# Kernel tuning notes

Hardware: AMD Instinct MI355X
Metric: run time of the kernel (lower is better)

The kernel has to match this reference:

```python
import jax, jax.numpy as jnp
import numpy as np

THRESHOLD = 0.5

def setup_inputs() -> dict:
    key = jax.random.key(0)
    x = jax.random.normal(key, (32, 2048, 1024), dtype=jnp.float32)
    return {"x": x}

def reference(x) -> jnp.ndarray:
    # x: [B, S, D]
    B, S, D = x.shape
    x_centered = x - jnp.mean(x, axis=1, keepdims=True)          # [B, S, D]
    # per-sample covariance: [B, D, D]
    cov = jnp.einsum('bsd,bse->bde', x_centered, x_centered) / (S - 1)
    std = jnp.sqrt(jnp.diagonal(cov, axis1=1, axis2=2))          # [B, D]
    corr = cov / (std[:, :, None] * std[:, None, :])             # [B, D, D]
    mask = jnp.abs(corr) > THRESHOLD                             # [B, D, D]
    eye = jnp.eye(D, dtype=bool)
    mask = mask & ~eye                                           # zero the diagonal
    # torch semantics: output[b, :, j] = 0 for every masked (b, i, j)
    col_kill = jnp.any(mask, axis=1)                             # [B, D]
    return x * (~col_kill)[:, None, :].astype(x.dtype)
```

## Files before the change

kernel.cpp:

```cpp
#include <hip/hip_runtime.h>
#include <stdint.h>

#define B_ 32
#define S_ 2048
#define D_ 1024

typedef __attribute__((ext_vector_type(16))) float f32x16;

__device__ __forceinline__ void async_copy16(const void* g, void* l) {
  __builtin_amdgcn_global_load_lds(
      (const __attribute__((address_space(1))) uint32_t*)g,
      (__attribute__((address_space(3))) uint32_t*)l, 16, 0, 0);
}

__device__ __forceinline__ int row_off(int m, int ch) {
  return m * 128 + ((ch ^ (m & 7)) << 4);
}

template <bool COPY>
__global__ __launch_bounds__(256) void prepass_kernel(const float* __restrict__ x,
                                                      uint8_t* __restrict__ xt,
                                                      float2* __restrict__ part,
                                                      float* __restrict__ out) {
  __shared__ float s_s[256 * 4];
  __shared__ float s_q[256 * 4];
  int dt = blockIdx.x;
  int slab = blockIdx.y;
  int b = blockIdx.z;
  int t = threadIdx.x;
  int q = t & 31;
  int e = t >> 5;
  int g = e >> 1, bh = e & 1;

  const size_t base = ((size_t)b * S_ + (size_t)slab * 128 + g * 32 + bh * 8) * D_ +
                      dt * 128 + q * 4;
  const float* xb = x + base;
  float4 r[16];
#pragma unroll
  for (int j = 0; j < 8; ++j) r[j] = *(const float4*)(xb + (size_t)j * D_);
#pragma unroll
  for (int j = 0; j < 8; ++j) r[8 + j] = *(const float4*)(xb + (size_t)(16 + j) * D_);

  if (COPY) {
    float* ob = out + base;
#pragma unroll
    for (int j = 0; j < 8; ++j) *(float4*)(ob + (size_t)j * D_) = r[j];
#pragma unroll
    for (int j = 0; j < 8; ++j) *(float4*)(ob + (size_t)(16 + j) * D_) = r[8 + j];
  }

  uint8_t* img = xt + (((size_t)b * 8 + dt) * 16 + slab) * 16384;
#pragma unroll
  for (int c = 0; c < 4; ++c) {
    float v[16];
#pragma unroll
    for (int j = 0; j < 16; ++j) v[j] = ((const float*)&r[j])[c];
    float ps = 0.f, pq = 0.f;
#pragma unroll
    for (int j = 0; j < 16; ++j) { ps += v[j]; pq += v[j] * v[j]; }
    s_s[t * 4 + c] = ps;
    s_q[t * 4 + c] = pq;
    uint32_t w0 = 0, w1 = 0, w2 = 0, w3 = 0;
    w0 = __builtin_amdgcn_cvt_pk_fp8_f32(v[0], v[1], w0, false);
    w0 = __builtin_amdgcn_cvt_pk_fp8_f32(v[2], v[3], w0, true);
    w1 = __builtin_amdgcn_cvt_pk_fp8_f32(v[4], v[5], w1, false);
    w1 = __builtin_amdgcn_cvt_pk_fp8_f32(v[6], v[7], w1, true);
    w2 = __builtin_amdgcn_cvt_pk_fp8_f32(v[8], v[9], w2, false);
    w2 = __builtin_amdgcn_cvt_pk_fp8_f32(v[10], v[11], w2, true);
    w3 = __builtin_amdgcn_cvt_pk_fp8_f32(v[12], v[13], w3, false);
    w3 = __builtin_amdgcn_cvt_pk_fp8_f32(v[14], v[15], w3, true);
    int m = 4 * q + c;
    *(uint4*)(img + row_off(m, (g << 1) | bh)) = make_uint4(w0, w1, w2, w3);
  }
  __syncthreads();
  if (t < 128) {
    int m = t, qq = m >> 2, cc = m & 3;
    float ss = 0.f, sq = 0.f;
#pragma unroll
    for (int ee = 0; ee < 8; ++ee) {
      ss += s_s[(qq + 32 * ee) * 4 + cc];
      sq += s_q[(qq + 32 * ee) * 4 + cc];
    }
    part[(size_t)slab * 32768 + b * 1024 + dt * 128 + m] = make_float2(ss, sq);
  }
}

__global__ void finalize_kernel(const float2* __restrict__ part,
                                float* __restrict__ meanB,
                                float* __restrict__ stdB) {
  int i = blockIdx.x * 256 + threadIdx.x;
  float s = 0.f, qv = 0.f;
#pragma unroll
  for (int sl = 0; sl < 16; ++sl) {
    float2 p = part[(size_t)sl * 32768 + i];
    s += p.x;
    qv += p.y;
  }
  float m = s * (1.0f / (float)S_);
  float var = (qv - s * m) * (1.0f / (float)(S_ - 1));
  meanB[i] = m;
  stdB[i] = sqrtf(fmaxf(var, 0.f));
}

__global__ __launch_bounds__(256) void gram_kernel(const uint8_t* __restrict__ xt,
                                                   const float* __restrict__ meanB,
                                                   const float* __restrict__ stdB,
                                                   int* __restrict__ colkill) {
  __shared__ uint8_t smA[16384];
  __shared__ uint8_t smB[16384];
  int b = blockIdx.y;
  int p = blockIdx.x;
  int i = 0;
  while (p >= 8 - i) { p -= 8 - i; ++i; }
  int j = i + p;

  int tid = threadIdx.x;
  int lane = tid & 63, wave = tid >> 6;
  int wm = wave & 1, wn = wave >> 1;
  int l31 = lane & 31, half = lane >> 5;

  f32x16 acc[2][2];
#pragma unroll
  for (int a = 0; a < 2; ++a)
#pragma unroll
    for (int c = 0; c < 2; ++c)
#pragma unroll
      for (int r = 0; r < 16; ++r) acc[a][c][r] = 0.f;

  const uint8_t* gA = xt + ((size_t)b * 8 + i) * 262144;
  const uint8_t* gB = xt + ((size_t)b * 8 + j) * 262144;
  bool diag = (i == j);

  for (int sl = 0; sl < 16; ++sl) {
    __syncthreads();
    const uint8_t* srcA = gA + (size_t)sl * 16384;
    for (int c = wave; c < 16; c += 4)
      async_copy16(srcA + c * 1024 + lane * 16, (void*)(smA + c * 1024));
    if (!diag) {
      const uint8_t* srcB = gB + (size_t)sl * 16384;
      for (int c = wave; c < 16; c += 4)
        async_copy16(srcB + c * 1024 + lane * 16, (void*)(smB + c * 1024));
    }
    __syncthreads();

    const uint8_t* bA = smA;
    const uint8_t* bB = diag ? smA : smB;
#pragma unroll
    for (int g = 0; g < 4; ++g) {
      ulonglong2 a0 = *(const ulonglong2*)(bA + row_off(wm * 64 + l31, (g << 1) | half));
      ulonglong2 a1 = *(const ulonglong2*)(bA + row_off(wm * 64 + 32 + l31, (g << 1) | half));
      ulonglong2 b0 = *(const ulonglong2*)(bB + row_off(wn * 64 + l31, (g << 1) | half));
      ulonglong2 b1 = *(const ulonglong2*)(bB + row_off(wn * 64 + 32 + l31, (g << 1) | half));
      acc[0][0] = __builtin_amdgcn_mfma_f32_32x32x16_fp8_fp8((long)a0.x, (long)b0.x, acc[0][0], 0, 0, 0);
      acc[0][1] = __builtin_amdgcn_mfma_f32_32x32x16_fp8_fp8((long)a0.x, (long)b1.x, acc[0][1], 0, 0, 0);
      acc[1][0] = __builtin_amdgcn_mfma_f32_32x32x16_fp8_fp8((long)a1.x, (long)b0.x, acc[1][0], 0, 0, 0);
      acc[1][1] = __builtin_amdgcn_mfma_f32_32x32x16_fp8_fp8((long)a1.x, (long)b1.x, acc[1][1], 0, 0, 0);
      acc[0][0] = __builtin_amdgcn_mfma_f32_32x32x16_fp8_fp8((long)a0.y, (long)b0.y, acc[0][0], 0, 0, 0);
      acc[0][1] = __builtin_amdgcn_mfma_f32_32x32x16_fp8_fp8((long)a0.y, (long)b1.y, acc[0][1], 0, 0, 0);
      acc[1][0] = __builtin_amdgcn_mfma_f32_32x32x16_fp8_fp8((long)a1.y, (long)b0.y, acc[1][0], 0, 0, 0);
      acc[1][1] = __builtin_amdgcn_mfma_f32_32x32x16_fp8_fp8((long)a1.y, (long)b1.y, acc[1][1], 0, 0, 0);
    }
  }

  const float* mb = meanB + b * D_;
  const float* sb = stdB + b * D_;
#pragma unroll
  for (int t = 0; t < 2; ++t) {
#pragma unroll
    for (int u = 0; u < 2; ++u) {
      int e = j * 128 + wn * 64 + u * 32 + l31;
      float me = mb[e], se05 = 0.5f * sb[e];
#pragma unroll
      for (int r = 0; r < 16; ++r) {
        int row = half * 4 + (r & 3) + 8 * (r >> 2);
        int d = i * 128 + wm * 64 + t * 32 + row;
        float cov = (acc[t][u][r] - (float)S_ * mb[d] * me) * (1.0f / (float)(S_ - 1));
        if (d != e && fabsf(cov) > se05 * sb[d]) {
          atomicOr(colkill + b * D_ + e, 1);
          atomicOr(colkill + b * D_ + d, 1);
        }
      }
    }
  }
}

__global__ void apply_kernel(const float* __restrict__ x,
                             const int* __restrict__ colkill,
                             float* __restrict__ out) {
  size_t idx = (size_t)blockIdx.x * 256 + threadIdx.x;
  const float4 v = ((const float4*)x)[idx];
  size_t e0 = idx * 4;
  int d = (int)(e0 & (D_ - 1));
  int b = (int)(e0 >> 21);
  const int4 k = *(const int4*)(colkill + b * D_ + d);
  float4 o;
  o.x = k.x ? 0.f : v.x;
  o.y = k.y ? 0.f : v.y;
  o.z = k.z ? 0.f : v.z;
  o.w = k.w ? 0.f : v.w;
  ((float4*)out)[idx] = o;
}

__global__ __launch_bounds__(256) void zerocol_kernel(const int* __restrict__ colkill,
                                                      float* __restrict__ out) {
  int bd = blockIdx.x * 256 + threadIdx.x;
  if (colkill[bd] == 0) return;
  int b = bd >> 10, d = bd & (D_ - 1);
  float* p = out + (size_t)b * S_ * D_ + d;
#pragma unroll 8
  for (int s = 0; s < S_; ++s) p[(size_t)s * D_] = 0.f;
}

extern "C" void kernel_launch(void* const* d_in, const int* in_sizes, int n_in,
                              void* d_out, int out_size, void* d_ws, size_t ws_size,
                              hipStream_t stream) {
  const float* x = (const float*)d_in[0];
  float* out = (float*)d_out;

  const size_t need = ((size_t)69 << 20);
  if (ws_size >= need) {
    uint8_t* xt = (uint8_t*)d_ws;
    float2* part = (float2*)((uint8_t*)d_ws + ((size_t)64 << 20));
    float* meanB = (float*)((uint8_t*)d_ws + ((size_t)68 << 20));
    float* stdB = meanB + 32768;
    int* colkill = (int*)(stdB + 32768);

    hipMemsetAsync(colkill, 0, 32768 * sizeof(int), stream);
    prepass_kernel<true><<<dim3(8, 16, 32), 256, 0, stream>>>(x, xt, part, out);
    finalize_kernel<<<128, 256, 0, stream>>>(part, meanB, stdB);
    gram_kernel<<<dim3(36, 32), 256, 0, stream>>>(xt, meanB, stdB, colkill);
    zerocol_kernel<<<128, 256, 0, stream>>>(colkill, out);
  } else {
    uint8_t* xt = (uint8_t*)d_out;
    float2* part = (float2*)d_ws;
    float* meanB = (float*)((uint8_t*)d_ws + (16 * 32768) * sizeof(float2));
    float* stdB = meanB + 32768;
    int* colkill = (int*)(stdB + 32768);

    hipMemsetAsync(colkill, 0, 32768 * sizeof(int), stream);
    prepass_kernel<false><<<dim3(8, 16, 32), 256, 0, stream>>>(x, xt, part, nullptr);
    finalize_kernel<<<128, 256, 0, stream>>>(part, meanB, stdB);
    gram_kernel<<<dim3(36, 32), 256, 0, stream>>>(xt, meanB, stdB, colkill);
    apply_kernel<<<65536, 256, 0, stream>>>(x, colkill, out);
  }
}
```

Before: 529.3 us.

## Double-buffer gram LDS loads, fuse stats finalize into gram, use nontemporal prepass I/O

```diff
diff --git a/kernel.cpp b/kernel.cpp
--- a/kernel.cpp
+++ b/kernel.cpp
@@ -6,6 +6,7 @@
 #define D_ 1024
 
 typedef __attribute__((ext_vector_type(16))) float f32x16;
+typedef __attribute__((ext_vector_type(4))) float f32x4;
 
 __device__ __forceinline__ void async_copy16(const void* g, void* l) {
   __builtin_amdgcn_global_load_lds(
@@ -34,19 +35,21 @@
 
   const size_t base = ((size_t)b * S_ + (size_t)slab * 128 + g * 32 + bh * 8) * D_ +
                       dt * 128 + q * 4;
-  const float* xb = x + base;
-  float4 r[16];
-#pragma unroll
-  for (int j = 0; j < 8; ++j) r[j] = *(const float4*)(xb + (size_t)j * D_);
-#pragma unroll
-  for (int j = 0; j < 8; ++j) r[8 + j] = *(const float4*)(xb + (size_t)(16 + j) * D_);
+  const f32x4* xb = (const f32x4*)(x + base);
+  f32x4 r[16];
+#pragma unroll
+  for (int j = 0; j < 8; ++j) r[j] = __builtin_nontemporal_load(xb + (size_t)j * (D_ / 4));
+#pragma unroll
+  for (int j = 0; j < 8; ++j)
+    r[8 + j] = __builtin_nontemporal_load(xb + (size_t)(16 + j) * (D_ / 4));
 
   if (COPY) {
-    float* ob = out + base;
-#pragma unroll
-    for (int j = 0; j < 8; ++j) *(float4*)(ob + (size_t)j * D_) = r[j];
-#pragma unroll
-    for (int j = 0; j < 8; ++j) *(float4*)(ob + (size_t)(16 + j) * D_) = r[8 + j];
+    f32x4* ob = (f32x4*)(out + base);
+#pragma unroll
+    for (int j = 0; j < 8; ++j) __builtin_nontemporal_store(r[j], ob + (size_t)j * (D_ / 4));
+#pragma unroll
+    for (int j = 0; j < 8; ++j)
+      __builtin_nontemporal_store(r[8 + j], ob + (size_t)(16 + j) * (D_ / 4));
   }
 
   uint8_t* img = xt + (((size_t)b * 8 + dt) * 16 + slab) * 16384;
@@ -54,7 +57,7 @@
   for (int c = 0; c < 4; ++c) {
     float v[16];
 #pragma unroll
-    for (int j = 0; j < 16; ++j) v[j] = ((const float*)&r[j])[c];
+    for (int j = 0; j < 16; ++j) v[j] = r[j][c];
     float ps = 0.f, pq = 0.f;
 #pragma unroll
     for (int j = 0; j < 16; ++j) { ps += v[j]; pq += v[j] * v[j]; }
@@ -85,29 +88,13 @@
   }
 }
 
-__global__ void finalize_kernel(const float2* __restrict__ part,
-                                float* __restrict__ meanB,
-                                float* __restrict__ stdB) {
-  int i = blockIdx.x * 256 + threadIdx.x;
-  float s = 0.f, qv = 0.f;
-#pragma unroll
-  for (int sl = 0; sl < 16; ++sl) {
-    float2 p = part[(size_t)sl * 32768 + i];
-    s += p.x;
-    qv += p.y;
-  }
-  float m = s * (1.0f / (float)S_);
-  float var = (qv - s * m) * (1.0f / (float)(S_ - 1));
-  meanB[i] = m;
-  stdB[i] = sqrtf(fmaxf(var, 0.f));
-}
-
 __global__ __launch_bounds__(256) void gram_kernel(const uint8_t* __restrict__ xt,
-                                                   const float* __restrict__ meanB,
-                                                   const float* __restrict__ stdB,
+                                                   const float2* __restrict__ part,
                                                    int* __restrict__ colkill) {
-  __shared__ uint8_t smA[16384];
-  __shared__ uint8_t smB[16384];
+  __shared__ uint8_t smA[2][16384];
+  __shared__ uint8_t smB[2][16384];
+  __shared__ float s_mean[256];
+  __shared__ float s_std[256];
   int b = blockIdx.y;
   int p = blockIdx.x;
   int i = 0;
@@ -118,33 +105,61 @@
   int lane = tid & 63, wave = tid >> 6;
   int wm = wave & 1, wn = wave >> 1;
   int l31 = lane & 31, half = lane >> 5;
-
-  f32x16 acc[2][2];
-#pragma unroll
-  for (int a = 0; a < 2; ++a)
-#pragma unroll
-    for (int c = 0; c < 2; ++c)
-#pragma unroll
-      for (int r = 0; r < 16; ++r) acc[a][c][r] = 0.f;
+  bool diag = (i == j);
 
   const uint8_t* gA = xt + ((size_t)b * 8 + i) * 262144;
   const uint8_t* gB = xt + ((size_t)b * 8 + j) * 262144;
-  bool diag = (i == j);
+
+  for (int c = wave; c < 16; c += 4)
+    async_copy16(gA + c * 1024 + lane * 16, (void*)(smA[0] + c * 1024));
+  if (!diag) {
+    for (int c = wave; c < 16; c += 4)
+      async_copy16(gB + c * 1024 + lane * 16, (void*)(smB[0] + c * 1024));
+  }
+
+  {
+    int dl = tid & 127;
+    int strip = (tid >> 7) ? j : i;
+    int d = strip * 128 + dl;
+    float s = 0.f, qv = 0.f;
+#pragma unroll
+    for (int sl = 0; sl < 16; ++sl) {
+      float2 pp = part[(size_t)sl * 32768 + b * 1024 + d];
+      s += pp.x;
+      qv += pp.y;
+    }
+    float m = s * (1.0f / (float)S_);
+    float var = (qv - s * m) * (1.0f / (float)(S_ - 1));
+    s_mean[tid] = m;
+    s_std[tid] = sqrtf(fmaxf(var, 0.f));
+  }
+
+  f32x16 acc[2][2];
+#pragma unroll
+  for (int a = 0; a < 2; ++a)
+#pragma unroll
+    for (int c = 0; c < 2; ++c)
+#pragma unroll
+      for (int r = 0; r < 16; ++r) acc[a][c][r] = 0.f;
+
+  __syncthreads();
 
   for (int sl = 0; sl < 16; ++sl) {
-    __syncthreads();
-    const uint8_t* srcA = gA + (size_t)sl * 16384;
-    for (int c = wave; c < 16; c += 4)
-      async_copy16(srcA + c * 1024 + lane * 16, (void*)(smA + c * 1024));
-    if (!diag) {
-      const uint8_t* srcB = gB + (size_t)sl * 16384;
+    int cur = sl & 1;
+    if (sl < 15) {
+      const uint8_t* srcA = gA + (size_t)(sl + 1) * 16384;
       for (int c = wave; c < 16; c += 4)
-        async_copy16(srcB + c * 1024 + lane * 16, (void*)(smB + c * 1024));
-    }
-    __syncthreads();
-
-    const uint8_t* bA = smA;
-    const uint8_t* bB = diag ? smA : smB;
+        async_copy16(srcA + c * 1024 + lane * 16, (void*)(smA[cur ^ 1] + c * 1024));
+      if (!diag) {
+        const uint8_t* srcB = gB + (size_t)(sl + 1) * 16384;
+        for (int c = wave; c < 16; c += 4)
+          async_copy16(srcB + c * 1024 + lane * 16, (void*)(smB[cur ^ 1] + c * 1024));
+      }
+    }
+    __builtin_amdgcn_sched_barrier(0);
+
+    const uint8_t* bA = smA[cur];
+    const uint8_t* bB = diag ? smA[cur] : smB[cur];
 #pragma unroll
     for (int g = 0; g < 4; ++g) {
       ulonglong2 a0 = *(const ulonglong2*)(bA + row_off(wm * 64 + l31, (g << 1) | half));
@@ -160,23 +175,28 @@
       acc[1][0] = __builtin_amdgcn_mfma_f32_32x32x16_fp8_fp8((long)a1.y, (long)b0.y, acc[1][0], 0, 0, 0);
       acc[1][1] = __builtin_amdgcn_mfma_f32_32x32x16_fp8_fp8((long)a1.y, (long)b1.y, acc[1][1], 0, 0, 0);
     }
-  }
-
-  const float* mb = meanB + b * D_;
-  const float* sb = stdB + b * D_;
+    __syncthreads();
+  }
+
+  const float* mbI = s_mean;
+  const float* sbI = s_std;
+  const float* mbJ = s_mean + 128;
+  const float* sbJ = s_std + 128;
 #pragma unroll
   for (int t = 0; t < 2; ++t) {
 #pragma unroll
     for (int u = 0; u < 2; ++u) {
-      int e = j * 128 + wn * 64 + u * 32 + l31;
-      float me = mb[e], se05 = 0.5f * sb[e];
+      int el = wn * 64 + u * 32 + l31;
+      int ee = j * 128 + el;
+      float me = mbJ[el], se05 = 0.5f * sbJ[el];
 #pragma unroll
       for (int r = 0; r < 16; ++r) {
         int row = half * 4 + (r & 3) + 8 * (r >> 2);
-        int d = i * 128 + wm * 64 + t * 32 + row;
-        float cov = (acc[t][u][r] - (float)S_ * mb[d] * me) * (1.0f / (float)(S_ - 1));
-        if (d != e && fabsf(cov) > se05 * sb[d]) {
-          atomicOr(colkill + b * D_ + e, 1);
+        int dl = wm * 64 + t * 32 + row;
+        int d = i * 128 + dl;
+        float cov = (acc[t][u][r] - (float)S_ * mbI[dl] * me) * (1.0f / (float)(S_ - 1));
+        if (d != ee && fabsf(cov) > se05 * sbI[dl]) {
+          atomicOr(colkill + b * D_ + ee, 1);
           atomicOr(colkill + b * D_ + d, 1);
         }
       }
@@ -221,26 +241,20 @@
   if (ws_size >= need) {
     uint8_t* xt = (uint8_t*)d_ws;
     float2* part = (float2*)((uint8_t*)d_ws + ((size_t)64 << 20));
-    float* meanB = (float*)((uint8_t*)d_ws + ((size_t)68 << 20));
-    float* stdB = meanB + 32768;
-    int* colkill = (int*)(stdB + 32768);
+    int* colkill = (int*)((uint8_t*)d_ws + ((size_t)68 << 20));
 
     hipMemsetAsync(colkill, 0, 32768 * sizeof(int), stream);
     prepass_kernel<true><<<dim3(8, 16, 32), 256, 0, stream>>>(x, xt, part, out);
-    finalize_kernel<<<128, 256, 0, stream>>>(part, meanB, stdB);
-    gram_kernel<<<dim3(36, 32), 256, 0, stream>>>(xt, meanB, stdB, colkill);
+    gram_kernel<<<dim3(36, 32), 256, 0, stream>>>(xt, part, colkill);
     zerocol_kernel<<<128, 256, 0, stream>>>(colkill, out);
   } else {
     uint8_t* xt = (uint8_t*)d_out;
     float2* part = (float2*)d_ws;
-    float* meanB = (float*)((uint8_t*)d_ws + (16 * 32768) * sizeof(float2));
-    float* stdB = meanB + 32768;
-    int* colkill = (int*)(stdB + 32768);
+    int* colkill = (int*)((uint8_t*)d_ws + (16 * 32768) * sizeof(float2));
 
     hipMemsetAsync(colkill, 0, 32768 * sizeof(int), stream);
     prepass_kernel<false><<<dim3(8, 16, 32), 256, 0, stream>>>(x, xt, part, nullptr);
-    finalize_kernel<<<128, 256, 0, stream>>>(part, meanB, stdB);
-    gram_kernel<<<dim3(36, 32), 256, 0, stream>>>(xt, meanB, stdB, colkill);
+    gram_kernel<<<dim3(36, 32), 256, 0, stream>>>(xt, part, colkill);
     apply_kernel<<<65536, 256, 0, stream>>>(x, colkill, out);
   }
 }
```

Measured after the change: 520.1 us. No clear change (-1.7%).
